# Performance work log

Measured on AMD Instinct MI355X. Metric: run time of the kernel, lower is better.

Reference implementation:

```python
import jax, jax.numpy as jnp
import numpy as np
from functools import partial

N_USERS = 30000
N_ENTITIES = 70000
N = N_USERS + N_ENTITIES
D = 64
N_EDGES = 1_600_000
EPS = 1e-12


def setup_inputs() -> dict:
    key = jax.random.key(0)
    ks = jax.random.split(key, 10)
    s = 1.0 / np.sqrt(D)  # xavier-like scale for weights
    return {
        "user_tab": jax.random.normal(ks[0], (N_USERS, D), jnp.float32) * 0.1,
        "entity_tab": jax.random.normal(ks[1], (N_ENTITIES, D), jnp.float32) * 0.1,
        "A_vals": jax.random.uniform(ks[2], (N_EDGES,), jnp.float32) / 16.0,  # ~row-normalized
        "W1_1": jax.random.normal(ks[3], (D, D), jnp.float32) * s,
        "b1_1": jnp.zeros((D,), jnp.float32),
        "W2_1": jax.random.normal(ks[4], (D, D), jnp.float32) * s,
        "b2_1": jnp.zeros((D,), jnp.float32),
        "W1_2": jax.random.normal(ks[5], (D, 32), jnp.float32) * s,
        "b1_2": jnp.zeros((32,), jnp.float32),
        "W2_2": jax.random.normal(ks[6], (D, 32), jnp.float32) * s,
        "b2_2": jnp.zeros((32,), jnp.float32),
        "A_rows": jax.random.randint(ks[7], (N_EDGES,), 0, N, jnp.int64 if jax.config.jax_enable_x64 else jnp.int32),
        "A_cols": jax.random.randint(ks[8], (N_EDGES,), 0, N, jnp.int64 if jax.config.jax_enable_x64 else jnp.int32),
    }


def _spmm(rows, cols, vals, x):
    # sparse A (COO) @ dense x : gather tail embeddings, scale, scatter-add to rows
    msgs = x[cols] * vals[:, None]            # [E, d]
    return jax.ops.segment_sum(msgs, rows, num_segments=N)


def _l2norm(x):
    n = jnp.sqrt(jnp.sum(x * x, axis=1, keepdims=True))
    return x / jnp.maximum(n, EPS)


def _bi_layer(ego, side, W1, b1, W2, b2):
    sum_e = jax.nn.leaky_relu((ego + side) @ W1 + b1)  # slope 0.01 = torch default
    bi_e = jax.nn.leaky_relu((ego * side) @ W2 + b2)
    return _l2norm(sum_e + bi_e)  # dropout p=0 (eval)


def reference(user_tab, entity_tab, A_vals, W1_1, b1_1, W2_1, b2_1,
              W1_2, b1_2, W2_2, b2_2, A_rows, A_cols):
    ego = jnp.concatenate([user_tab, entity_tab], axis=0)  # [N, 64]
    all_embed = [ego]
    # layer 1: 64 -> 64
    side = _spmm(A_rows, A_cols, A_vals, ego)
    ego = _bi_layer(ego, side, W1_1, b1_1, W2_1, b2_1)
    all_embed.append(ego)
    # layer 2: 64 -> 32
    side = _spmm(A_rows, A_cols, A_vals, ego)
    ego = _bi_layer(ego, side, W1_2, b1_2, W2_2, b2_2)
    all_embed.append(ego)
    return jnp.concatenate(all_embed, axis=1)  # [N, 160]; split [n_users, n_entities] downstream
```

## Files before the change

### kernel.cpp

```cpp
#include <hip/hip_runtime.h>
#include <hip/hip_bf16.h>
#include <string.h>

#define N_USERS 30000
#define N_NODES 100000
#define DIM 64
#define N_EDGES 1600000
#define ROWS_PER_BUCK 256
#define NB ((N_NODES + ROWS_PER_BUCK - 1) / ROWS_PER_BUCK)
#define CHUNK 8192
#define NBLK_B ((N_EDGES + CHUNK - 1) / CHUNK)
#define BUCK_SLACK 2048
#define E_ALLOC (N_EDGES + NB * BUCK_SLACK)
#define STAGE_CAP 5120
#define GCAP 64

typedef __hip_bfloat16 bf16;
typedef __attribute__((ext_vector_type(8))) short short8;
typedef __attribute__((ext_vector_type(4))) float floatx4;

__device__ __forceinline__ float b2f(bf16 v) { return __bfloat162float(v); }
__device__ __forceinline__ bf16 f2b(float v) { return __float2bfloat16(v); }
__device__ __forceinline__ unsigned short fbits(float v) {
    bf16 b = f2b(v); unsigned short u; memcpy(&u, &b, 2); return u;
}
__device__ __forceinline__ float ubf(unsigned u) {
    return __uint_as_float(u << 16);
}

__device__ __forceinline__ float ld(const void* p, int i, int f32) {
    return f32 ? ((const float*)p)[i] : b2f(((const bf16*)p)[i]);
}
__device__ __forceinline__ void st(void* p, int i, float v, int f32) {
    if (f32) ((float*)p)[i] = v; else ((bf16*)p)[i] = f2b(v);
}
__device__ __forceinline__ unsigned short wbits(const void* p, int i, int f32) {
    return f32 ? fbits(((const float*)p)[i]) : ((const unsigned short*)p)[i];
}

__global__ void k_detect(const void* user, const void* ent, const void* vals,
                         const void* W, int* flags, int* bsize) {
    int t = threadIdx.x;
    for (int i = t; i < NB; i += 128) bsize[i] = 0;
    const void* ps[4] = { user, ent, vals, W };
    int k = t >> 5, i = t & 31;
    float v = ((const float*)ps[k])[i];
    int ok = (v == v && fabsf(v) <= 1e4f) ? 1 : 0;
    ok += __shfl_xor(ok, 1, 64);
    ok += __shfl_xor(ok, 2, 64);
    ok += __shfl_xor(ok, 4, 64);
    ok += __shfl_xor(ok, 8, 64);
    ok += __shfl_xor(ok, 16, 64);
    if ((t & 31) == 0) flags[k] = (ok >= 16) ? 1 : 0;
}

__global__ __launch_bounds__(256) void k_prepw(
    const void* W1_1, const void* b1_1, const void* W2_1, const void* b2_1,
    const void* W1_2, const void* b1_2, const void* W2_2, const void* b2_2,
    short8* wf1, float2* wsb1, short8* wf2, float* wsb2,
    const int* flags) {
    int t = threadIdx.x;
    int w = t >> 6, quad = (t >> 4) & 3, sub = t & 15;
    int fw = flags[3];
    short8 f0, f1, f2, f3;
#pragma unroll
    for (int j = 0; j < 8; ++j) {
        int k0 = quad * 8 + j, n = w * 16 + sub;
        f0[j] = (short)wbits(W1_1, k0 * 64 + n, fw);
        f1[j] = (short)wbits(W1_1, (k0 + 32) * 64 + n, fw);
        f2[j] = (short)wbits(W2_1, k0 * 64 + n, fw);
        f3[j] = (short)wbits(W2_1, (k0 + 32) * 64 + n, fw);
    }
    short8* p = wf1 + ((w * 4 + quad) * 16 + sub) * 4;
    p[0] = f0; p[1] = f1; p[2] = f2; p[3] = f3;
    if (quad == 0)
        wsb1[w * 16 + sub] = make_float2(ld(b1_1, w * 16 + sub, fw),
                                         ld(b2_1, w * 16 + sub, fw));
    int path = w >> 1, nbase = (w & 1) * 16;
    const void* W = path ? W2_2 : W1_2;
    const void* bb = path ? b2_2 : b1_2;
    short8 g0, g1;
#pragma unroll
    for (int j = 0; j < 8; ++j) {
        int k0 = quad * 8 + j, n = nbase + sub;
        g0[j] = (short)wbits(W, k0 * 32 + n, fw);
        g1[j] = (short)wbits(W, (k0 + 32) * 32 + n, fw);
    }
    short8* q = wf2 + ((w * 4 + quad) * 16 + sub) * 2;
    q[0] = g0; q[1] = g1;
    if (quad == 0) wsb2[w * 16 + sub] = ld(bb, nbase + sub, fw);
}

__global__ __launch_bounds__(256) void k_hista(const int* __restrict__ rows,
                                               int* __restrict__ cnt_table,
                                               int* __restrict__ bsize) {
    __shared__ int h[NB];
    int t = threadIdx.x, blk = blockIdx.x;
    for (int b = t; b < NB; b += 256) h[b] = 0;
    __syncthreads();
    int base = blk * CHUNK + t * 4;
#pragma unroll
    for (int it = 0; it < 8; ++it) {
        int e = base + it * 1024;
        if (e < N_EDGES) {
            int4 r = *(const int4*)&rows[e];
            atomicAdd(&h[r.x >> 8], 1);
            atomicAdd(&h[r.y >> 8], 1);
            atomicAdd(&h[r.z >> 8], 1);
            atomicAdd(&h[r.w >> 8], 1);
        }
    }
    __syncthreads();
    for (int b = t; b < NB; b += 256) {
        int v = h[b];
        cnt_table[blk * NB + b] = v;
        if (v) atomicAdd(&bsize[b], v);
    }
}

__global__ __launch_bounds__(512) void k_bscan(const int* __restrict__ bsize,
                                               int* __restrict__ bbase) {
    __shared__ int lds[512];
    int t = threadIdx.x;
    int v = (t < NB) ? (((bsize[t] + 3) & ~3) + BUCK_SLACK) : 0;
    lds[t] = v;
    __syncthreads();
    for (int off = 1; off < 512; off <<= 1) {
        int u = (t >= off) ? lds[t - off] : 0;
        __syncthreads();
        lds[t] += u;
        __syncthreads();
    }
    if (t <= NB) bbase[t] = (t == 0) ? 0 : lds[t - 1];
}

__global__ __launch_bounds__(256) void k_bscan2(int* __restrict__ cnt_table,
                                                const int* __restrict__ bbase) {
    __shared__ int lds[256];
    int t = threadIdx.x, b = blockIdx.x;
    int v = (t < NBLK_B) ? cnt_table[t * NB + b] : 0;
    lds[t] = v;
    __syncthreads();
    for (int off = 1; off < 256; off <<= 1) {
        int u = (t >= off) ? lds[t - off] : 0;
        __syncthreads();
        lds[t] += u;
        __syncthreads();
    }
    if (t < NBLK_B) cnt_table[t * NB + b] = bbase[b] + lds[t] - v;
}

__global__ __launch_bounds__(256) void k_bscatter2(
    const int* __restrict__ rows, const int* __restrict__ cols,
    const void* __restrict__ vals, const int* __restrict__ cnt_table,
    int2* __restrict__ bpack, const int* __restrict__ flags) {
    __shared__ int cur[NB];
    int t = threadIdx.x, blk = blockIdx.x;
    int fv = flags[2];
    for (int b = t; b < NB; b += 256) cur[b] = cnt_table[blk * NB + b];
    __syncthreads();
    int base = blk * CHUNK + t * 4;
#pragma unroll
    for (int it = 0; it < 8; ++it) {
        int e = base + it * 1024;
        if (e < N_EDGES) {
            int4 r = *(const int4*)&rows[e];
            int4 c = *(const int4*)&cols[e];
            float v0, v1, v2, v3;
            if (fv) {
                float4 vv = *(const float4*)((const float*)vals + e);
                v0 = vv.x; v1 = vv.y; v2 = vv.z; v3 = vv.w;
            } else {
                const bf16* bp = (const bf16*)vals + e;
                v0 = b2f(bp[0]); v1 = b2f(bp[1]); v2 = b2f(bp[2]); v3 = b2f(bp[3]);
            }
            int p0 = atomicAdd(&cur[r.x >> 8], 1);
            int p1 = atomicAdd(&cur[r.y >> 8], 1);
            int p2 = atomicAdd(&cur[r.z >> 8], 1);
            int p3 = atomicAdd(&cur[r.w >> 8], 1);
            bpack[p0] = make_int2(c.x | ((r.x & 255) << 17), __float_as_int(v0));
            bpack[p1] = make_int2(c.y | ((r.y & 255) << 17), __float_as_int(v1));
            bpack[p2] = make_int2(c.z | ((r.z & 255) << 17), __float_as_int(v2));
            bpack[p3] = make_int2(c.w | ((r.w & 255) << 17), __float_as_int(v3));
        }
    }
}

__global__ __launch_bounds__(256) void k_place2(
    const int* __restrict__ bsize, const int* __restrict__ bbase,
    const int2* __restrict__ bpack, int2* __restrict__ epack,
    int* __restrict__ row_start, int* __restrict__ row_end) {
    __shared__ __align__(16) int2 stage[STAGE_CAP];
    __shared__ int rcnt[ROWS_PER_BUCK];
    __shared__ int scan_lds[ROWS_PER_BUCK];
    __shared__ int rstart[ROWS_PER_BUCK];
    __shared__ int cur[ROWS_PER_BUCK];
    int t = threadIdx.x, b = blockIdx.x;
    int n = bsize[b];
    int gstart = bbase[b];
    rcnt[t] = 0;
    __syncthreads();
    for (int i = t; i < n; i += 256) {
        int2 p = bpack[gstart + i];
        if (i < STAGE_CAP) stage[i] = p;
        atomicAdd(&rcnt[(p.x >> 17) & 255], 1);
    }
    __syncthreads();
    int c = rcnt[t];
    int cp = (c + 3) & ~3;
    int g = cp;
    g = max(g, __shfl_xor(g, 1, 64));
    g = max(g, __shfl_xor(g, 2, 64));
    scan_lds[t] = g;
    __syncthreads();
    for (int off = 1; off < 256; off <<= 1) {
        int u = (t >= off) ? scan_lds[t - off] : 0;
        __syncthreads();
        scan_lds[t] += u;
        __syncthreads();
    }
    int rs_ = gstart + scan_lds[t] - g;
    rstart[t] = rs_;
    cur[t] = rs_;
    int node = b * ROWS_PER_BUCK + t;
    if (node < N_NODES) {
        row_start[node] = rs_;
        row_end[node] = rs_ + g;
    }
    __syncthreads();
    for (int i = t; i < n; i += 256) {
        int2 p = (i < STAGE_CAP) ? stage[i] : bpack[gstart + i];
        int r = (p.x >> 17) & 255;
        int pos = atomicAdd(&cur[r], 1);
        epack[pos] = make_int2(p.x & 0x1FFFF, p.y);
    }
    __syncthreads();
    int pend = rstart[t] + g;
    for (int pos = cur[t]; pos < pend; ++pos) epack[pos] = make_int2(0, 0);
}

__global__ void k_init(const void* __restrict__ user, const void* __restrict__ ent,
                       void* __restrict__ out, bf16* __restrict__ xb0,
                       const int* __restrict__ flags) {
    int i = blockIdx.x * blockDim.x + threadIdx.x;
    if (i >= N_NODES * DIM) return;
    int fo = flags[0], fe = flags[1];
    int n = i >> 6, d = i & 63;
    float v = (n < N_USERS) ? ld(user, i, fo) : ld(ent, i - N_USERS * DIM, fe);
    st(out, n * 160 + d, v, fo);
    xb0[i] = f2b(v);
}

#define G8_LOAD(r) \
    int b##r = (r * gstep + ei) >> 1; \
    int4 qa##r = lq4[b##r], qb##r = lq4[b##r + 1]; \
    int4 qc##r = lq4[b##r + 2], qd##r = lq4[b##r + 3];

#define G8_ISSUE(r) \
    unsigned g##r##0 = xu[qa##r.x * 64 + lane]; \
    unsigned g##r##1 = xu[qa##r.z * 64 + lane]; \
    unsigned g##r##2 = xu[qb##r.x * 64 + lane]; \
    unsigned g##r##3 = xu[qb##r.z * 64 + lane]; \
    unsigned g##r##4 = xu[qc##r.x * 64 + lane]; \
    unsigned g##r##5 = xu[qc##r.z * 64 + lane]; \
    unsigned g##r##6 = xu[qd##r.x * 64 + lane]; \
    unsigned g##r##7 = xu[qd##r.z * 64 + lane];

#define G8_FMA(r) \
    ea##r += __int_as_float(qa##r.y) * ubf(g##r##0); \
    ea##r += __int_as_float(qa##r.w) * ubf(g##r##1); \
    ea##r += __int_as_float(qb##r.y) * ubf(g##r##2); \
    ea##r += __int_as_float(qb##r.w) * ubf(g##r##3); \
    ea##r += __int_as_float(qc##r.y) * ubf(g##r##4); \
    ea##r += __int_as_float(qc##r.w) * ubf(g##r##5); \
    ea##r += __int_as_float(qd##r.y) * ubf(g##r##6); \
    ea##r += __int_as_float(qd##r.w) * ubf(g##r##7);

#define G4_LOAD(r) \
    int tb##r = (r * gstep + ei) >> 1; \
    int4 ua##r = lq4[tb##r], ub##r = lq4[tb##r + 1];

#define G4_ISSUE(r) \
    unsigned h##r##0 = xu[ua##r.x * 64 + lane]; \
    unsigned h##r##1 = xu[ua##r.z * 64 + lane]; \
    unsigned h##r##2 = xu[ub##r.x * 64 + lane]; \
    unsigned h##r##3 = xu[ub##r.z * 64 + lane];

#define G4_FMA(r) \
    ea##r += __int_as_float(ua##r.y) * ubf(h##r##0); \
    ea##r += __int_as_float(ua##r.w) * ubf(h##r##1); \
    ea##r += __int_as_float(ub##r.y) * ubf(h##r##2); \
    ea##r += __int_as_float(ub##r.w) * ubf(h##r##3);

#define FB_ROW_DECL(r) \
    int ej##r = rs_a[r] >> 1; \
    int4 eA##r = ep4[ej##r]; \
    int4 eB##r = ep4[ej##r + 1];

#define FB_ISSUE(r) \
    unsigned eg##r##0 = xu[eA##r.x * 64 + lane]; \
    unsigned eg##r##1 = xu[eA##r.z * 64 + lane]; \
    unsigned eg##r##2 = xu[eB##r.x * 64 + lane]; \
    unsigned eg##r##3 = xu[eB##r.z * 64 + lane];

#define FB_ADV(r) \
    int4 nA##r = ep4[ej##r + 2]; \
    int4 nB##r = ep4[ej##r + 3]; \
    ej##r += 2;

#define FB_FMA(r) \
    ea##r += __int_as_float(eA##r.y) * ubf(eg##r##0); \
    ea##r += __int_as_float(eA##r.w) * ubf(eg##r##1); \
    ea##r += __int_as_float(eB##r.y) * ubf(eg##r##2); \
    ea##r += __int_as_float(eB##r.w) * ubf(eg##r##3); \
    eA##r = nA##r; eB##r = nB##r;

#define GATHER_BODY \
    float ea0 = 0.f, ea1 = 0.f, ea2 = 0.f, ea3 = 0.f; \
    if (emx <= GCAP) { \
        { \
            const int2* eps = (const int2*)epack + rs0; \
            int tot = emx << 2; \
            for (int i = lane; i < tot; i += 64) lq[i] = eps[i]; \
        } \
        int ei = 0; \
        for (; ei + 8 <= emx; ei += 8) { \
            G8_LOAD(0) G8_LOAD(1) G8_LOAD(2) G8_LOAD(3) \
            G8_ISSUE(0) G8_ISSUE(1) G8_ISSUE(2) G8_ISSUE(3) \
            G8_FMA(0) G8_FMA(1) G8_FMA(2) G8_FMA(3) \
        } \
        if (ei < emx) { \
            G4_LOAD(0) G4_LOAD(1) G4_LOAD(2) G4_LOAD(3) \
            G4_ISSUE(0) G4_ISSUE(1) G4_ISSUE(2) G4_ISSUE(3) \
            G4_FMA(0) G4_FMA(1) G4_FMA(2) G4_FMA(3) \
        } \
    } else { \
        const int4* ep4 = (const int4*)epack; \
        int rs_a[4] = { rsv.x, rsv.y, rsv.z, rsv.w }; \
        FB_ROW_DECL(0) FB_ROW_DECL(1) FB_ROW_DECL(2) FB_ROW_DECL(3) \
        for (int ei = 0; ei < emx; ei += 4) { \
            FB_ISSUE(0) FB_ISSUE(1) FB_ISSUE(2) FB_ISSUE(3) \
            FB_ADV(0) FB_ADV(1) FB_ADV(2) FB_ADV(3) \
            FB_FMA(0) FB_FMA(1) FB_FMA(2) FB_FMA(3) \
        } \
    }

__global__ __launch_bounds__(256) void k_layer1(
    const short8* __restrict__ wf1, const float2* __restrict__ wsb1,
    void* __restrict__ out, const int* __restrict__ row_start,
    const int* __restrict__ row_end,
    const int2* __restrict__ epack, const bf16* __restrict__ xt,
    bf16* __restrict__ xn, const int* __restrict__ flags) {
    __shared__ __align__(16) int2 lq_lds[4][4 * GCAP];
    __shared__ __align__(16) unsigned short hp_lds[16][72];
    __shared__ __align__(16) unsigned short hm_lds[16][72];
    __shared__ __align__(16) float ssq_lds[16][4];
    int t = threadIdx.x, lane = t & 63, w = t >> 6;
    int sub = lane & 15, quad = lane >> 4;
    int fo = flags[0];
    int rbase = blockIdx.x * 16 + w * 4;
    const unsigned short* xu = (const unsigned short*)xt;

    int4 rsv = *(const int4*)&row_start[rbase];
    int rs0 = __builtin_amdgcn_readfirstlane(rsv.x);
    int emx = __builtin_amdgcn_readfirstlane(row_end[rbase] - rsv.x);
    int gstep = emx;
    int2* lq = lq_lds[w];
    const int4* lq4 = (const int4*)lq;
    GATHER_BODY
    {
        float s[4] = { ea0, ea1, ea2, ea3 };
#pragma unroll
        for (int r = 0; r < 4; ++r) {
            float h = ld(out, (rbase + r) * 160 + lane, fo);
            hp_lds[w * 4 + r][lane] = fbits(h + s[r]);
            hm_lds[w * 4 + r][lane] = fbits(h * s[r]);
        }
    }
    __syncthreads();

    short8 Ap0 = *(const short8*)((const char*)hp_lds + sub * 144 + quad * 16);
    short8 Ap1 = *(const short8*)((const char*)hp_lds + sub * 144 + 64 + quad * 16);
    short8 Am0 = *(const short8*)((const char*)hm_lds + sub * 144 + quad * 16);
    short8 Am1 = *(const short8*)((const char*)hm_lds + sub * 144 + 64 + quad * 16);

    const short8* wfp = wf1 + ((w * 4 + quad) * 16 + sub) * 4;
    short8 Bw10 = wfp[0], Bw11 = wfp[1], Bw20 = wfp[2], Bw21 = wfp[3];
    float2 bb12 = wsb1[w * 16 + sub];
    float bias1 = bb12.x, bias2 = bb12.y;
    int wbase = w * 16;

    floatx4 c1; c1[0] = bias1; c1[1] = bias1; c1[2] = bias1; c1[3] = bias1;
    floatx4 c2; c2[0] = bias2; c2[1] = bias2; c2[2] = bias2; c2[3] = bias2;
    c1 = __builtin_amdgcn_mfma_f32_16x16x32_bf16(Ap0, Bw10, c1, 0, 0, 0);
    c1 = __builtin_amdgcn_mfma_f32_16x16x32_bf16(Ap1, Bw11, c1, 0, 0, 0);
    c2 = __builtin_amdgcn_mfma_f32_16x16x32_bf16(Am0, Bw20, c2, 0, 0, 0);
    c2 = __builtin_amdgcn_mfma_f32_16x16x32_bf16(Am1, Bw21, c2, 0, 0, 0);

    float v[4], sp[4];
#pragma unroll
    for (int r = 0; r < 4; ++r) {
        float s1 = c1[r], s2 = c2[r];
        s1 = s1 > 0.f ? s1 : 0.01f * s1;
        s2 = s2 > 0.f ? s2 : 0.01f * s2;
        v[r] = s1 + s2;
        float sq = v[r] * v[r];
        sq += __shfl_xor(sq, 1, 64);
        sq += __shfl_xor(sq, 2, 64);
        sq += __shfl_xor(sq, 4, 64);
        sq += __shfl_xor(sq, 8, 64);
        sp[r] = sq;
    }
    if (sub == 0) {
#pragma unroll
        for (int r = 0; r < 4; ++r) ssq_lds[quad * 4 + r][w] = sp[r];
    }
    __syncthreads();
#pragma unroll
    for (int r = 0; r < 4; ++r) {
        int row = quad * 4 + r;
        floatx4 ps = *(const floatx4*)&ssq_lds[row][0];
        float ss = ps[0] + ps[1] + ps[2] + ps[3];
        float o = v[r] * (1.0f / fmaxf(sqrtf(ss), 1e-12f));
        int n = blockIdx.x * 16 + row;
        st(out, n * 160 + 64 + wbase + sub, o, fo);
        xn[n * 64 + wbase + sub] = f2b(o);
    }
}

__global__ __launch_bounds__(256) void k_layer2(
    const short8* __restrict__ wf2, const float* __restrict__ wsb2,
    void* __restrict__ out, const int* __restrict__ row_start,
    const int* __restrict__ row_end,
    const int2* __restrict__ epack, const bf16* __restrict__ xt,
    const int* __restrict__ flags) {
    __shared__ __align__(16) int2 lq_lds[4][4 * GCAP];
    __shared__ __align__(16) unsigned short hp_lds[16][72];
    __shared__ __align__(16) unsigned short hm_lds[16][72];
    __shared__ __align__(16) float bi_lds[16][32];
    __shared__ __align__(16) float ssq_lds[16][2];
    int t = threadIdx.x, lane = t & 63, w = t >> 6;
    int sub = lane & 15, quad = lane >> 4;
    int fo = flags[0];
    int rbase = blockIdx.x * 16 + w * 4;
    const unsigned short* xu = (const unsigned short*)xt;

    int4 rsv = *(const int4*)&row_start[rbase];
    int rs0 = __builtin_amdgcn_readfirstlane(rsv.x);
    int emx = __builtin_amdgcn_readfirstlane(row_end[rbase] - rsv.x);
    int gstep = emx;
    int2* lq = lq_lds[w];
    const int4* lq4 = (const int4*)lq;
    GATHER_BODY
    {
        float s[4] = { ea0, ea1, ea2, ea3 };
#pragma unroll
        for (int r = 0; r < 4; ++r) {
            float h = ld(out, (rbase + r) * 160 + 64 + lane, fo);
            hp_lds[w * 4 + r][lane] = fbits(h + s[r]);
            hm_lds[w * 4 + r][lane] = fbits(h * s[r]);
        }
    }
    __syncthreads();

    int path = w >> 1;
    int nbase = (w & 1) * 16;
    const unsigned short(*hl)[72] = path ? hm_lds : hp_lds;
    short8 Af0 = *(const short8*)((const char*)hl + sub * 144 + quad * 16);
    short8 Af1 = *(const short8*)((const char*)hl + sub * 144 + 64 + quad * 16);

    const short8* wfp = wf2 + ((w * 4 + quad) * 16 + sub) * 2;
    short8 Bf0 = wfp[0], Bf1 = wfp[1];
    float bias = wsb2[w * 16 + sub];

    floatx4 c; c[0] = bias; c[1] = bias; c[2] = bias; c[3] = bias;
    c = __builtin_amdgcn_mfma_f32_16x16x32_bf16(Af0, Bf0, c, 0, 0, 0);
    c = __builtin_amdgcn_mfma_f32_16x16x32_bf16(Af1, Bf1, c, 0, 0, 0);

    float T[4];
#pragma unroll
    for (int r = 0; r < 4; ++r) {
        float x = c[r];
        T[r] = x > 0.f ? x : 0.01f * x;
        if (path == 1) bi_lds[quad * 4 + r][nbase + sub] = T[r];
    }
    __syncthreads();

    float v[4], sp[4];
#pragma unroll
    for (int r = 0; r < 4; ++r) {
        v[r] = T[r] + bi_lds[quad * 4 + r][nbase + sub];
        float sq = v[r] * v[r];
        sq += __shfl_xor(sq, 1, 64);
        sq += __shfl_xor(sq, 2, 64);
        sq += __shfl_xor(sq, 4, 64);
        sq += __shfl_xor(sq, 8, 64);
        sp[r] = sq;
    }
    if (path == 0 && sub == 0) {
#pragma unroll
        for (int r = 0; r < 4; ++r) ssq_lds[quad * 4 + r][w & 1] = sp[r];
    }
    __syncthreads();
    if (path == 0) {
#pragma unroll
        for (int r = 0; r < 4; ++r) {
            int row = quad * 4 + r;
            float ss = ssq_lds[row][0] + ssq_lds[row][1];
            float o = v[r] * (1.0f / fmaxf(sqrtf(ss), 1e-12f));
            int n = blockIdx.x * 16 + row;
            st(out, n * 160 + 128 + nbase + sub, o, fo);
        }
    }
}

extern "C" void kernel_launch(void* const* d_in, const int* in_sizes, int n_in,
                              void* d_out, int out_size, void* d_ws, size_t ws_size,
                              hipStream_t stream) {
    const void* user = d_in[0];
    const void* ent  = d_in[1];
    const void* vals = d_in[2];
    const void* W1_1 = d_in[3];
    const void* b1_1 = d_in[4];
    const void* W2_1 = d_in[5];
    const void* b2_1 = d_in[6];
    const void* W1_2 = d_in[7];
    const void* b1_2 = d_in[8];
    const void* W2_2 = d_in[9];
    const void* b2_2 = d_in[10];
    const int* rows  = (const int*)d_in[11];
    const int* cols  = (const int*)d_in[12];

    char* w = (char*)d_ws;
    int* flags     = (int*)w;    w += 256;
    int* bsize     = (int*)w;    w += 2048;
    int* bbase     = (int*)w;    w += 2048;
    short8* wf1    = (short8*)w; w += 16384;
    float2* wsb1   = (float2*)w; w += 512;
    short8* wf2    = (short8*)w; w += 8192;
    float* wsb2    = (float*)w;  w += 256;
    int* row_start = (int*)w;    w += 400128;
    int* row_end   = (int*)w;    w += 400128;
    int2* epack    = (int2*)w;   w += (size_t)E_ALLOC * 8;
    bf16* xb0      = (bf16*)w;   w += (size_t)N_NODES * DIM * 2;
    bf16* xb1      = (bf16*)w;
    int* cnt_table = (int*)epack;
    int2* bpack    = (int2*)xb0;

    k_detect<<<1, 128, 0, stream>>>(user, ent, vals, W1_1, flags, bsize);
    k_prepw<<<1, 256, 0, stream>>>(W1_1, b1_1, W2_1, b2_1, W1_2, b1_2, W2_2, b2_2,
                                   wf1, wsb1, wf2, wsb2, flags);
    k_hista<<<NBLK_B, 256, 0, stream>>>(rows, cnt_table, bsize);
    k_bscan<<<1, 512, 0, stream>>>(bsize, bbase);
    k_bscan2<<<NB, 256, 0, stream>>>(cnt_table, bbase);
    k_bscatter2<<<NBLK_B, 256, 0, stream>>>(rows, cols, vals, cnt_table, bpack, flags);
    k_place2<<<NB, 256, 0, stream>>>(bsize, bbase, bpack, epack, row_start, row_end);
    k_init<<<(N_NODES * DIM + 255) / 256, 256, 0, stream>>>(user, ent, d_out, xb0, flags);
    k_layer1<<<N_NODES / 16, 256, 0, stream>>>(wf1, wsb1, d_out, row_start, row_end, epack, xb0, xb1, flags);
    k_layer2<<<N_NODES / 16, 256, 0, stream>>>(wf2, wsb2, d_out, row_start, row_end, epack, xb1, flags);
}
```

Before: 309.2 us.

## Sort rows by degree within buckets to balance gather groups, pre-scale column indices

Within each 256-row bucket, rows are now rank-sorted by padded edge count and grouped four at a time. Each wavefront group pads only to the maximum degree among similar rows rather than among four adjacent rows, which cuts the padding work in the gather loops. Layer kernels read group start/length and a permutation to scatter results back to the original node order. Column indices are stored pre-shifted as byte offsets so the gathers avoid a multiply, and the edge-binning chunk size is halved. In exchange it adds an O(256) rank sort per bucket, indirect output writes, and a launch over padded node counts.

```diff
diff --git a/kernel.cpp b/kernel.cpp
--- a/kernel.cpp
+++ b/kernel.cpp
@@ -8,7 +8,8 @@
 #define N_EDGES 1600000
 #define ROWS_PER_BUCK 256
 #define NB ((N_NODES + ROWS_PER_BUCK - 1) / ROWS_PER_BUCK)
-#define CHUNK 8192
+#define NGRP (NB * 64)
+#define CHUNK 4096
 #define NBLK_B ((N_EDGES + CHUNK - 1) / CHUNK)
 #define BUCK_SLACK 2048
 #define E_ALLOC (N_EDGES + NB * BUCK_SLACK)
@@ -100,7 +101,7 @@
     __syncthreads();
     int base = blk * CHUNK + t * 4;
 #pragma unroll
-    for (int it = 0; it < 8; ++it) {
+    for (int it = 0; it < 4; ++it) {
         int e = base + it * 1024;
         if (e < N_EDGES) {
             int4 r = *(const int4*)&rows[e];
@@ -134,14 +135,14 @@
     if (t <= NB) bbase[t] = (t == 0) ? 0 : lds[t - 1];
 }
 
-__global__ __launch_bounds__(256) void k_bscan2(int* __restrict__ cnt_table,
+__global__ __launch_bounds__(512) void k_bscan2(int* __restrict__ cnt_table,
                                                 const int* __restrict__ bbase) {
-    __shared__ int lds[256];
+    __shared__ int lds[512];
     int t = threadIdx.x, b = blockIdx.x;
     int v = (t < NBLK_B) ? cnt_table[t * NB + b] : 0;
     lds[t] = v;
     __syncthreads();
-    for (int off = 1; off < 256; off <<= 1) {
+    for (int off = 1; off < 512; off <<= 1) {
         int u = (t >= off) ? lds[t - off] : 0;
         __syncthreads();
         lds[t] += u;
@@ -161,7 +162,7 @@
     __syncthreads();
     int base = blk * CHUNK + t * 4;
 #pragma unroll
-    for (int it = 0; it < 8; ++it) {
+    for (int it = 0; it < 4; ++it) {
         int e = base + it * 1024;
         if (e < N_EDGES) {
             int4 r = *(const int4*)&rows[e];
@@ -189,11 +190,13 @@
 __global__ __launch_bounds__(256) void k_place2(
     const int* __restrict__ bsize, const int* __restrict__ bbase,
     const int2* __restrict__ bpack, int2* __restrict__ epack,
-    int* __restrict__ row_start, int* __restrict__ row_end) {
+    int* __restrict__ grp_start, int* __restrict__ grp_len,
+    int* __restrict__ perm) {
     __shared__ __align__(16) int2 stage[STAGE_CAP];
     __shared__ int rcnt[ROWS_PER_BUCK];
-    __shared__ int scan_lds[ROWS_PER_BUCK];
-    __shared__ int rstart[ROWS_PER_BUCK];
+    __shared__ int skey[ROWS_PER_BUCK];
+    __shared__ int scn[ROWS_PER_BUCK];
+    __shared__ int sbr[ROWS_PER_BUCK];
     __shared__ int cur[ROWS_PER_BUCK];
     int t = threadIdx.x, b = blockIdx.x;
     int n = bsize[b];
@@ -208,34 +211,42 @@
     __syncthreads();
     int c = rcnt[t];
     int cp = (c + 3) & ~3;
-    int g = cp;
-    g = max(g, __shfl_xor(g, 1, 64));
-    g = max(g, __shfl_xor(g, 2, 64));
-    scan_lds[t] = g;
+    int key = (cp << 8) | t;
+    __syncthreads();
+    rcnt[t] = key;
+    __syncthreads();
+    int rank = 0;
+    for (int u = 0; u < 256; ++u) rank += (rcnt[u] < key) ? 1 : 0;
+    skey[rank] = key;
+    __syncthreads();
+    int gq = skey[t | 3] >> 8;
+    scn[t] = gq;
     __syncthreads();
     for (int off = 1; off < 256; off <<= 1) {
-        int u = (t >= off) ? scan_lds[t - off] : 0;
+        int u = (t >= off) ? scn[t - off] : 0;
         __syncthreads();
-        scan_lds[t] += u;
+        scn[t] += u;
         __syncthreads();
     }
-    int rs_ = gstart + scan_lds[t] - g;
-    rstart[t] = rs_;
-    cur[t] = rs_;
-    int node = b * ROWS_PER_BUCK + t;
-    if (node < N_NODES) {
-        row_start[node] = rs_;
-        row_end[node] = rs_ + g;
+    sbr[t] = gstart + scn[t] - gq;
+    __syncthreads();
+    cur[t] = sbr[rank];
+    int rowp = skey[t] & 255;
+    int gid = b * 64 + (t >> 2);
+    perm[gid * 4 + (t & 3)] = b * 256 + rowp;
+    if ((t & 3) == 0) {
+        grp_start[gid] = sbr[t];
+        grp_len[gid] = skey[t | 3] >> 8;
     }
     __syncthreads();
     for (int i = t; i < n; i += 256) {
         int2 p = (i < STAGE_CAP) ? stage[i] : bpack[gstart + i];
         int r = (p.x >> 17) & 255;
         int pos = atomicAdd(&cur[r], 1);
-        epack[pos] = make_int2(p.x & 0x1FFFF, p.y);
-    }
-    __syncthreads();
-    int pend = rstart[t] + g;
+        epack[pos] = make_int2((p.x & 0x1FFFF) << 7, p.y);
+    }
+    __syncthreads();
+    int pend = sbr[rank] + (skey[rank | 3] >> 8);
     for (int pos = cur[t]; pos < pend; ++pos) epack[pos] = make_int2(0, 0);
 }
 
@@ -252,19 +263,19 @@
 }
 
 #define G8_LOAD(r) \
-    int b##r = (r * gstep + ei) >> 1; \
+    int b##r = (r * emx + ei) >> 1; \
     int4 qa##r = lq4[b##r], qb##r = lq4[b##r + 1]; \
     int4 qc##r = lq4[b##r + 2], qd##r = lq4[b##r + 3];
 
 #define G8_ISSUE(r) \
-    unsigned g##r##0 = xu[qa##r.x * 64 + lane]; \
-    unsigned g##r##1 = xu[qa##r.z * 64 + lane]; \
-    unsigned g##r##2 = xu[qb##r.x * 64 + lane]; \
-    unsigned g##r##3 = xu[qb##r.z * 64 + lane]; \
-    unsigned g##r##4 = xu[qc##r.x * 64 + lane]; \
-    unsigned g##r##5 = xu[qc##r.z * 64 + lane]; \
-    unsigned g##r##6 = xu[qd##r.x * 64 + lane]; \
-    unsigned g##r##7 = xu[qd##r.z * 64 + lane];
+    unsigned g##r##0 = *(const unsigned short*)(xbp + (unsigned)qa##r.x); \
+    unsigned g##r##1 = *(const unsigned short*)(xbp + (unsigned)qa##r.z); \
+    unsigned g##r##2 = *(const unsigned short*)(xbp + (unsigned)qb##r.x); \
+    unsigned g##r##3 = *(const unsigned short*)(xbp + (unsigned)qb##r.z); \
+    unsigned g##r##4 = *(const unsigned short*)(xbp + (unsigned)qc##r.x); \
+    unsigned g##r##5 = *(const unsigned short*)(xbp + (unsigned)qc##r.z); \
+    unsigned g##r##6 = *(const unsigned short*)(xbp + (unsigned)qd##r.x); \
+    unsigned g##r##7 = *(const unsigned short*)(xbp + (unsigned)qd##r.z);
 
 #define G8_FMA(r) \
     ea##r += __int_as_float(qa##r.y) * ubf(g##r##0); \
@@ -277,14 +288,14 @@
     ea##r += __int_as_float(qd##r.w) * ubf(g##r##7);
 
 #define G4_LOAD(r) \
-    int tb##r = (r * gstep + ei) >> 1; \
+    int tb##r = (r * emx + ei) >> 1; \
     int4 ua##r = lq4[tb##r], ub##r = lq4[tb##r + 1];
 
 #define G4_ISSUE(r) \
-    unsigned h##r##0 = xu[ua##r.x * 64 + lane]; \
-    unsigned h##r##1 = xu[ua##r.z * 64 + lane]; \
-    unsigned h##r##2 = xu[ub##r.x * 64 + lane]; \
-    unsigned h##r##3 = xu[ub##r.z * 64 + lane];
+    unsigned h##r##0 = *(const unsigned short*)(xbp + (unsigned)ua##r.x); \
+    unsigned h##r##1 = *(const unsigned short*)(xbp + (unsigned)ua##r.z); \
+    unsigned h##r##2 = *(const unsigned short*)(xbp + (unsigned)ub##r.x); \
+    unsigned h##r##3 = *(const unsigned short*)(xbp + (unsigned)ub##r.z);
 
 #define G4_FMA(r) \
     ea##r += __int_as_float(ua##r.y) * ubf(h##r##0); \
@@ -293,15 +304,15 @@
     ea##r += __int_as_float(ub##r.w) * ubf(h##r##3);
 
 #define FB_ROW_DECL(r) \
-    int ej##r = rs_a[r] >> 1; \
+    int ej##r = (rs0 + r * emx) >> 1; \
     int4 eA##r = ep4[ej##r]; \
     int4 eB##r = ep4[ej##r + 1];
 
 #define FB_ISSUE(r) \
-    unsigned eg##r##0 = xu[eA##r.x * 64 + lane]; \
-    unsigned eg##r##1 = xu[eA##r.z * 64 + lane]; \
-    unsigned eg##r##2 = xu[eB##r.x * 64 + lane]; \
-    unsigned eg##r##3 = xu[eB##r.z * 64 + lane];
+    unsigned eg##r##0 = *(const unsigned short*)(xbp + (unsigned)eA##r.x); \
+    unsigned eg##r##1 = *(const unsigned short*)(xbp + (unsigned)eA##r.z); \
+    unsigned eg##r##2 = *(const unsigned short*)(xbp + (unsigned)eB##r.x); \
+    unsigned eg##r##3 = *(const unsigned short*)(xbp + (unsigned)eB##r.z);
 
 #define FB_ADV(r) \
     int4 nA##r = ep4[ej##r + 2]; \
@@ -336,7 +347,6 @@
         } \
     } else { \
         const int4* ep4 = (const int4*)epack; \
-        int rs_a[4] = { rsv.x, rsv.y, rsv.z, rsv.w }; \
         FB_ROW_DECL(0) FB_ROW_DECL(1) FB_ROW_DECL(2) FB_ROW_DECL(3) \
         for (int ei = 0; ei < emx; ei += 4) { \
             FB_ISSUE(0) FB_ISSUE(1) FB_ISSUE(2) FB_ISSUE(3) \
@@ -347,8 +357,8 @@
 
 __global__ __launch_bounds__(256) void k_layer1(
     const short8* __restrict__ wf1, const float2* __restrict__ wsb1,
-    void* __restrict__ out, const int* __restrict__ row_start,
-    const int* __restrict__ row_end,
+    void* __restrict__ out, const int* __restrict__ grp_start,
+    const int* __restrict__ grp_len, const int* __restrict__ perm,
     const int2* __restrict__ epack, const bf16* __restrict__ xt,
     bf16* __restrict__ xn, const int* __restrict__ flags) {
     __shared__ __align__(16) int2 lq_lds[4][4 * GCAP];
@@ -358,21 +368,22 @@
     int t = threadIdx.x, lane = t & 63, w = t >> 6;
     int sub = lane & 15, quad = lane >> 4;
     int fo = flags[0];
-    int rbase = blockIdx.x * 16 + w * 4;
-    const unsigned short* xu = (const unsigned short*)xt;
-
-    int4 rsv = *(const int4*)&row_start[rbase];
-    int rs0 = __builtin_amdgcn_readfirstlane(rsv.x);
-    int emx = __builtin_amdgcn_readfirstlane(row_end[rbase] - rsv.x);
-    int gstep = emx;
+    int gid = blockIdx.x * 4 + w;
+    const char* xbp = (const char*)xt + (lane << 1);
+
+    int rs0 = __builtin_amdgcn_readfirstlane(grp_start[gid]);
+    int emx = __builtin_amdgcn_readfirstlane(grp_len[gid]);
+    int4 pn = *(const int4*)&perm[gid * 4];
     int2* lq = lq_lds[w];
     const int4* lq4 = (const int4*)lq;
     GATHER_BODY
     {
         float s[4] = { ea0, ea1, ea2, ea3 };
+        int nd[4] = { pn.x, pn.y, pn.z, pn.w };
 #pragma unroll
         for (int r = 0; r < 4; ++r) {
-            float h = ld(out, (rbase + r) * 160 + lane, fo);
+            int node = (nd[r] < N_NODES) ? nd[r] : 0;
+            float h = ld(out, node * 160 + lane, fo);
             hp_lds[w * 4 + r][lane] = fbits(h + s[r]);
             hm_lds[w * 4 + r][lane] = fbits(h * s[r]);
         }
@@ -416,22 +427,25 @@
         for (int r = 0; r < 4; ++r) ssq_lds[quad * 4 + r][w] = sp[r];
     }
     __syncthreads();
+    const int* pblk = perm + blockIdx.x * 16;
 #pragma unroll
     for (int r = 0; r < 4; ++r) {
         int row = quad * 4 + r;
         floatx4 ps = *(const floatx4*)&ssq_lds[row][0];
         float ss = ps[0] + ps[1] + ps[2] + ps[3];
         float o = v[r] * (1.0f / fmaxf(sqrtf(ss), 1e-12f));
-        int n = blockIdx.x * 16 + row;
-        st(out, n * 160 + 64 + wbase + sub, o, fo);
-        xn[n * 64 + wbase + sub] = f2b(o);
+        int n = pblk[row];
+        if (n < N_NODES) {
+            st(out, n * 160 + 64 + wbase + sub, o, fo);
+            xn[n * 64 + wbase + sub] = f2b(o);
+        }
     }
 }
 
 __global__ __launch_bounds__(256) void k_layer2(
     const short8* __restrict__ wf2, const float* __restrict__ wsb2,
-    void* __restrict__ out, const int* __restrict__ row_start,
-    const int* __restrict__ row_end,
+    void* __restrict__ out, const int* __restrict__ grp_start,
+    const int* __restrict__ grp_len, const int* __restrict__ perm,
     const int2* __restrict__ epack, const bf16* __restrict__ xt,
     const int* __restrict__ flags) {
     __shared__ __align__(16) int2 lq_lds[4][4 * GCAP];
@@ -442,21 +456,22 @@
     int t = threadIdx.x, lane = t & 63, w = t >> 6;
     int sub = lane & 15, quad = lane >> 4;
     int fo = flags[0];
-    int rbase = blockIdx.x * 16 + w * 4;
-    const unsigned short* xu = (const unsigned short*)xt;
-
-    int4 rsv = *(const int4*)&row_start[rbase];
-    int rs0 = __builtin_amdgcn_readfirstlane(rsv.x);
-    int emx = __builtin_amdgcn_readfirstlane(row_end[rbase] - rsv.x);
-    int gstep = emx;
+    int gid = blockIdx.x * 4 + w;
+    const char* xbp = (const char*)xt + (lane << 1);
+
+    int rs0 = __builtin_amdgcn_readfirstlane(grp_start[gid]);
+    int emx = __builtin_amdgcn_readfirstlane(grp_len[gid]);
+    int4 pn = *(const int4*)&perm[gid * 4];
     int2* lq = lq_lds[w];
     const int4* lq4 = (const int4*)lq;
     GATHER_BODY
     {
         float s[4] = { ea0, ea1, ea2, ea3 };
+        int nd[4] = { pn.x, pn.y, pn.z, pn.w };
 #pragma unroll
         for (int r = 0; r < 4; ++r) {
-            float h = ld(out, (rbase + r) * 160 + 64 + lane, fo);
+            int node = (nd[r] < N_NODES) ? nd[r] : 0;
+            float h = ld(out, node * 160 + 64 + lane, fo);
             hp_lds[w * 4 + r][lane] = fbits(h + s[r]);
             hm_lds[w * 4 + r][lane] = fbits(h * s[r]);
         }
@@ -503,13 +518,14 @@
     }
     __syncthreads();
     if (path == 0) {
+        const int* pblk = perm + blockIdx.x * 16;
 #pragma unroll
         for (int r = 0; r < 4; ++r) {
             int row = quad * 4 + r;
             float ss = ssq_lds[row][0] + ssq_lds[row][1];
             float o = v[r] * (1.0f / fmaxf(sqrtf(ss), 1e-12f));
-            int n = blockIdx.x * 16 + row;
-            st(out, n * 160 + 128 + nbase + sub, o, fo);
+            int n = pblk[row];
+            if (n < N_NODES) st(out, n * 160 + 128 + nbase + sub, o, fo);
         }
     }
 }
@@ -539,8 +555,9 @@
     float2* wsb1   = (float2*)w; w += 512;
     short8* wf2    = (short8*)w; w += 8192;
     float* wsb2    = (float*)w;  w += 256;
-    int* row_start = (int*)w;    w += 400128;
-    int* row_end   = (int*)w;    w += 400128;
+    int* grp_start = (int*)w;    w += 100352;
+    int* grp_len   = (int*)w;    w += 100352;
+    int* perm      = (int*)w;    w += 400384;
     int2* epack    = (int2*)w;   w += (size_t)E_ALLOC * 8;
     bf16* xb0      = (bf16*)w;   w += (size_t)N_NODES * DIM * 2;
     bf16* xb1      = (bf16*)w;
@@ -552,10 +569,10 @@
                                    wf1, wsb1, wf2, wsb2, flags);
     k_hista<<<NBLK_B, 256, 0, stream>>>(rows, cnt_table, bsize);
     k_bscan<<<1, 512, 0, stream>>>(bsize, bbase);
-    k_bscan2<<<NB, 256, 0, stream>>>(cnt_table, bbase);
+    k_bscan2<<<NB, 512, 0, stream>>>(cnt_table, bbase);
     k_bscatter2<<<NBLK_B, 256, 0, stream>>>(rows, cols, vals, cnt_table, bpack, flags);
-    k_place2<<<NB, 256, 0, stream>>>(bsize, bbase, bpack, epack, row_start, row_end);
+    k_place2<<<NB, 256, 0, stream>>>(bsize, bbase, bpack, epack, grp_start, grp_len, perm);
     k_init<<<(N_NODES * DIM + 255) / 256, 256, 0, stream>>>(user, ent, d_out, xb0, flags);
-    k_layer1<<<N_NODES / 16, 256, 0, stream>>>(wf1, wsb1, d_out, row_start, row_end, epack, xb0, xb1, flags);
-    k_layer2<<<N_NODES / 16, 256, 0, stream>>>(wf2, wsb2, d_out, row_start, row_end, epack, xb1, flags);
-}
+    k_layer1<<<NB * 16, 256, 0, stream>>>(wf1, wsb1, d_out, grp_start, grp_len, perm, epack, xb0, xb1, flags);
+    k_layer2<<<NB * 16, 256, 0, stream>>>(wf2, wsb2, d_out, grp_start, grp_len, perm, epack, xb1, flags);
+}
```

After: 321.4 us. 1.04x slower.
